# Optimization experiments

Measured on AMD Instinct MI355X. Metric: run time of the kernel, lower is better.

Reference implementation:

```python
import jax, jax.numpy as jnp
import numpy as np

DIM = 1024
H = 16          # query heads
HKV = 4         # kv heads
HD = DIM // H   # head_dim = 64
B = 8           # equal-length docs
S = 1024        # tokens per doc
N = B * S       # total tokens
ROPE_BASE = 10000.0


def _rms_norm(x, scale):
    eps = jnp.asarray(jnp.finfo(x.dtype).eps, x.dtype)
    inv = jax.lax.rsqrt(jnp.mean(x * x, axis=-1, keepdims=True) + eps)
    return x * inv * scale


def _rope(x, cos, sin):
    # x: [N, h, HD]; cos/sin: [N, 1, HD//2]
    half = x.shape[-1] // 2
    x1, x2 = x[..., :half], x[..., half:]
    return jnp.concatenate((x1 * cos + x2 * sin, -x1 * sin + x2 * cos), axis=-1)


def setup_inputs() -> dict:
    key = jax.random.key(0)
    ks = jax.random.split(key, 8)
    x = jax.random.normal(ks[0], (N, DIM), dtype=jnp.float32)
    Wq = jax.random.normal(ks[1], (DIM, DIM), dtype=jnp.float32) * (DIM ** -0.5)
    Wk = jax.random.normal(ks[2], (HKV * HD, DIM), dtype=jnp.float32) * (DIM ** -0.5)
    Wv = jax.random.normal(ks[3], (HKV * HD, DIM), dtype=jnp.float32) * (DIM ** -0.5)
    Wproj = jax.random.normal(ks[4], (DIM, DIM), dtype=jnp.float32) * (DIM ** -0.5)
    q_gain = jnp.full((H,), 1.0, dtype=jnp.float32)
    q_scale = jnp.asarray(1.0, dtype=jnp.float32)  # q RMSNorm scale
    k_scale = jnp.asarray(1.0, dtype=jnp.float32)  # k RMSNorm scale
    # rotary tables per Rotary.prepare_positions (positions reset per doc)
    cu_seqlens = jnp.arange(B + 1, dtype=jnp.int32) * S
    positions = jnp.tile(jnp.arange(S, dtype=jnp.float32), B)  # [N]
    inv_freq = 1.0 / (ROPE_BASE ** (jnp.arange(0, HD, 2, dtype=jnp.float32) / HD))
    freqs = positions[:, None] * inv_freq[None, :]  # [N, HD//2]
    rotary_cos = jnp.cos(freqs)[:, None, :]
    rotary_sin = jnp.sin(freqs)[:, None, :]
    return {
        "x": x, "Wq": Wq, "Wk": Wk, "Wv": Wv, "Wproj": Wproj,
        "q_gain": q_gain, "q_scale": q_scale, "k_scale": k_scale,
        "rotary_cos": rotary_cos, "rotary_sin": rotary_sin,
        "cu_seqlens": cu_seqlens, "max_doc_len": S,
    }


def reference(x, Wq, Wk, Wv, Wproj, q_gain, q_scale, k_scale,
              rotary_cos, rotary_sin, cu_seqlens, max_doc_len):
    n_tokens, dim = x.shape
    q = (x @ Wq.T).reshape(n_tokens, H, HD)
    k = (x @ Wk.T).reshape(n_tokens, HKV, HD)
    v = (x @ Wv.T).reshape(n_tokens, HKV, HD)
    q = _rms_norm(q, q_scale)
    k = _rms_norm(k, k_scale)
    q = _rope(q, rotary_cos, rotary_sin)
    k = _rope(k, rotary_cos, rotary_sin)
    q = q * q_gain[None, :, None]
    # equal-length docs -> [B, S, h, HD]; GQA: repeat kv heads
    rep = H // HKV
    qb = q.reshape(B, S, H, HD)
    kb = jnp.repeat(k.reshape(B, S, HKV, HD), rep, axis=2)
    vb = jnp.repeat(v.reshape(B, S, HKV, HD), rep, axis=2)
    scale = HD ** -0.5
    scores = jnp.einsum('bqhd,bkhd->bhqk', qb, kb) * scale  # [B,H,S,S]
    causal = jnp.tril(jnp.ones((S, S), dtype=bool))
    scores = jnp.where(causal[None, None], scores, jnp.asarray(-jnp.inf, scores.dtype))
    attn = jax.nn.softmax(scores, axis=-1)
    y = jnp.einsum('bhqk,bkhd->bqhd', attn, vb).reshape(n_tokens, dim)
    return y @ Wproj.T
```

## Files before the change

kernel.cpp:

```cpp
#include <hip/hip_runtime.h>
#include <hip/hip_bf16.h>


typedef __bf16 bf16x8 __attribute__((ext_vector_type(8)));
typedef float f32x4 __attribute__((ext_vector_type(4)));

__device__ __forceinline__ void async16(const void* g, void* l) {
  __builtin_amdgcn_global_load_lds((const __attribute__((address_space(1))) void*)g,
                                   (__attribute__((address_space(3))) void*)l, 16, 0, 0);
}

__device__ __forceinline__ unsigned short f2bfu(float x) {
  __hip_bfloat16 h = __float2bfloat16(x);
  return __builtin_bit_cast(unsigned short, h);
}

__global__ __launch_bounds__(256) void castall(
    const float4* __restrict__ x, const float4* __restrict__ Wq,
    const float4* __restrict__ Wk, const float4* __restrict__ Wv,
    const float4* __restrict__ Wp,
    ushort4* __restrict__ xb, ushort4* __restrict__ w1b, ushort4* __restrict__ wpb) {
  int i = blockIdx.x * 256 + threadIdx.x;
  const float4* src;
  ushort4* dst;
  if (i < 2097152)      { src = x + i;             dst = xb + i; }
  else if (i < 2359296) { src = Wq + (i - 2097152); dst = w1b + (i - 2097152); }
  else if (i < 2424832) { src = Wk + (i - 2359296); dst = w1b + (i - 2097152); }
  else if (i < 2490368) { src = Wv + (i - 2424832); dst = w1b + (i - 2097152); }
  else                  { src = Wp + (i - 2490368); dst = wpb + (i - 2490368); }
  float4 v = *src;
  ushort4 o;
  o.x = f2bfu(v.x); o.y = f2bfu(v.y); o.z = f2bfu(v.z); o.w = f2bfu(v.w);
  *dst = o;
}

__global__ __launch_bounds__(256, 3) void gemm_qkv(
    const __hip_bfloat16* __restrict__ A,
    const __hip_bfloat16* __restrict__ Bm,
    const float* __restrict__ cosb, const float* __restrict__ sinb,
    const float* __restrict__ qgain, const float* __restrict__ qscale,
    const float* __restrict__ kscale,
    __hip_bfloat16* __restrict__ Qo,
    __hip_bfloat16* __restrict__ Ko,
    __hip_bfloat16* __restrict__ Vt)
{
  __shared__ __align__(16) unsigned short As[128 * 32];
  __shared__ __align__(16) unsigned short Bs[128 * 32];
  const int tid = threadIdx.x;
  const int wave = tid >> 6, lane = tid & 63;
  const int quad = lane >> 4, l15 = lane & 15;
  const int bn = blockIdx.x, bm = blockIdx.y;
  const int wm = (wave >> 1) * 64, wn = (wave & 1) * 64;
  const int srow = lane >> 2, scol = (lane & 3) * 8;
  const int K = 1024;

  f32x4 acc[4][4] = {};

  const __hip_bfloat16* Ab = A + (size_t)bm * 128 * K;
  const __hip_bfloat16* Bb = Bm + (size_t)bn * 128 * K;

  for (int kt = 0; kt < K; kt += 32) {
    __syncthreads();
#pragma unroll
    for (int c = 0; c < 2; c++) {
      const int ch = wave * 2 + c;
      async16(Ab + (size_t)(ch * 16 + srow) * K + kt + scol, &As[ch * 512]);
      async16(Bb + (size_t)(ch * 16 + srow) * K + kt + scol, &Bs[ch * 512]);
    }
    __syncthreads();
    bf16x8 af[4], bfr[4];
#pragma unroll
    for (int mt = 0; mt < 4; mt++)
      af[mt] = *(const bf16x8*)&As[(wm + mt * 16 + l15) * 32 + quad * 8];
#pragma unroll
    for (int nt = 0; nt < 4; nt++)
      bfr[nt] = *(const bf16x8*)&Bs[(wn + nt * 16 + l15) * 32 + quad * 8];
#pragma unroll
    for (int mt = 0; mt < 4; mt++)
#pragma unroll
      for (int nt = 0; nt < 4; nt++)
        acc[mt][nt] = __builtin_amdgcn_mfma_f32_16x16x32_bf16(af[mt], bfr[nt], acc[mt][nt], 0, 0, 0);
  }

  const int hg = bn * 2 + (wn >> 6);
  const int tokbase = bm * 128 + wm;

  if (hg >= 20) {
    const int hv = hg - 20;
    const int bb = tokbase >> 10;
    const int sbase = (tokbase & 1023) + quad * 4;
    unsigned short* vt = (unsigned short*)Vt;
#pragma unroll
    for (int nt = 0; nt < 4; nt++) {
      const size_t rowoff = ((size_t)((bb * 4 + hv) * 64 + nt * 16 + l15)) * 1024;
#pragma unroll
      for (int mt = 0; mt < 4; mt++) {
        ushort4 pk;
        unsigned short* pp = (unsigned short*)&pk;
#pragma unroll
        for (int r = 0; r < 4; r++) pp[r] = f2bfu(acc[mt][nt][r]);
        *(ushort4*)&vt[rowoff + sbase + mt * 16] = pk;
      }
    }
  } else {
    const bool isq = hg < 16;
    const float scale = isq ? qscale[0] : kscale[0];
    const float gain = isq ? qgain[hg] : 1.0f;
    const float sg = scale * gain;
#pragma unroll
    for (int mt = 0; mt < 4; mt++) {
      float inv[4];
#pragma unroll
      for (int r = 0; r < 4; r++) {
        float ss = acc[mt][0][r] * acc[mt][0][r] + acc[mt][1][r] * acc[mt][1][r] +
                   acc[mt][2][r] * acc[mt][2][r] + acc[mt][3][r] * acc[mt][3][r];
#pragma unroll
        for (int off = 1; off < 16; off <<= 1) ss += __shfl_xor(ss, off);
        inv[r] = rsqrtf(ss * (1.0f / 64.0f) + 1.1920929e-07f) * sg;
      }
#pragma unroll
      for (int r = 0; r < 4; r++) {
        const int tok = tokbase + mt * 16 + quad * 4 + r;
        const float c0 = cosb[tok * 32 + l15], c1 = cosb[tok * 32 + 16 + l15];
        const float s0 = sinb[tok * 32 + l15], s1 = sinb[tok * 32 + 16 + l15];
        const float v0 = acc[mt][0][r] * inv[r];
        const float v1 = acc[mt][1][r] * inv[r];
        const float v2 = acc[mt][2][r] * inv[r];
        const float v3 = acc[mt][3][r] * inv[r];
        const float o0 = v0 * c0 + v2 * s0;
        const float o1 = v1 * c1 + v3 * s1;
        const float o2 = -v0 * s0 + v2 * c0;
        const float o3 = -v1 * s1 + v3 * c1;
        __hip_bfloat16* base = isq ? (Qo + (size_t)tok * 1024 + hg * 64)
                                   : (Ko + (size_t)tok * 256 + (hg - 16) * 64);
        base[l15]      = __float2bfloat16(o0);
        base[16 + l15] = __float2bfloat16(o1);
        base[32 + l15] = __float2bfloat16(o2);
        base[48 + l15] = __float2bfloat16(o3);
      }
    }
  }
}

__global__ __launch_bounds__(256, 4) void gemm_p(
    const __hip_bfloat16* __restrict__ A,
    const __hip_bfloat16* __restrict__ Bm,
    float* __restrict__ C)
{
  __shared__ __align__(16) unsigned short As[128 * 32];
  __shared__ __align__(16) unsigned short Bs[64 * 32];
  const int tid = threadIdx.x;
  const int wave = tid >> 6, lane = tid & 63;
  const int quad = lane >> 4, l15 = lane & 15;
  const int bn = blockIdx.x, bm = blockIdx.y;
  const int wm = wave * 32;
  const int srow = lane >> 2, scol = (lane & 3) * 8;
  const int K = 1024;

  f32x4 acc[2][4] = {};

  const __hip_bfloat16* Ab = A + (size_t)bm * 128 * K;
  const __hip_bfloat16* Bb = Bm + (size_t)bn * 64 * K;

  for (int kt = 0; kt < K; kt += 32) {
    __syncthreads();
#pragma unroll
    for (int c = 0; c < 2; c++) {
      const int ch = wave * 2 + c;
      async16(Ab + (size_t)(ch * 16 + srow) * K + kt + scol, &As[ch * 512]);
    }
    async16(Bb + (size_t)(wave * 16 + srow) * K + kt + scol, &Bs[wave * 512]);
    __syncthreads();
    bf16x8 af[2], bfr[4];
#pragma unroll
    for (int mt = 0; mt < 2; mt++)
      af[mt] = *(const bf16x8*)&As[(wm + mt * 16 + l15) * 32 + quad * 8];
#pragma unroll
    for (int nt = 0; nt < 4; nt++)
      bfr[nt] = *(const bf16x8*)&Bs[(nt * 16 + l15) * 32 + quad * 8];
#pragma unroll
    for (int mt = 0; mt < 2; mt++)
#pragma unroll
      for (int nt = 0; nt < 4; nt++)
        acc[mt][nt] = __builtin_amdgcn_mfma_f32_16x16x32_bf16(af[mt], bfr[nt], acc[mt][nt], 0, 0, 0);
  }

#pragma unroll
  for (int mt = 0; mt < 2; mt++)
#pragma unroll
    for (int nt = 0; nt < 4; nt++)
#pragma unroll
      for (int r = 0; r < 4; r++) {
        const int row = bm * 128 + wm + mt * 16 + quad * 4 + r;
        const int col = bn * 64 + nt * 16 + l15;
        C[(size_t)row * 1024 + col] = acc[mt][nt][r];
      }
}

__global__ __launch_bounds__(256, 3) void attn(
    const __hip_bfloat16* __restrict__ Q,
    const __hip_bfloat16* __restrict__ Kk,
    const __hip_bfloat16* __restrict__ Vt,
    __hip_bfloat16* __restrict__ Y)
{
  __shared__ __align__(16) unsigned short Kb[2][4096];
  __shared__ __align__(16) unsigned short Vb[2][4096];
  __shared__ __align__(16) unsigned short Pm[4][32 * 72];
  __shared__ float Lsh[4][32];

  const int xx = blockIdx.x;
  const int qh = (xx & 1) ? (xx >> 1) : (31 - (xx >> 1));
  const int kvh = blockIdx.y, b = blockIdx.z;
  const int tid = threadIdx.x;
  const int wave = tid >> 6, lane = tid & 63;
  const int quad = lane >> 4, l15 = lane & 15;
  const int h = kvh * 4 + wave;
  const int tok0 = b * 1024 + qh * 32;
  const int m0 = (qh & 1) * 32;
  const int nkt = (qh >> 1) + 1;

  const int srow = lane >> 2;
  const int scol = (lane & 3) * 8;

  bf16x8 qf[2][2];
#pragma unroll
  for (int mt = 0; mt < 2; mt++)
#pragma unroll
    for (int kc = 0; kc < 2; kc++)
      qf[mt][kc] = *(const bf16x8*)(Q + (size_t)(tok0 + mt * 16 + l15) * 1024 +
                                    h * 64 + kc * 32 + quad * 8);

  auto issue = [&](int kt, unsigned short* Ks, unsigned short* Vs) {
#pragma unroll
    for (int c = 0; c < 4; c++) {
      const int ch = wave * 4 + c;
      const int v = ch >> 3;
      const int ch8 = ch & 7;
      const int kc = ch8 >> 2, grp = ch8 & 3;
      if (v == 0)
        async16(Kk + (size_t)(b * 1024 + kt * 64 + grp * 16 + srow) * 256 + kvh * 64 + kc * 32 + scol,
                Ks + kc * 2048 + grp * 512 + lane * 8);
      else
        async16(Vt + ((size_t)((b * 4 + kvh) * 64 + grp * 16 + srow)) * 1024 + kt * 64 + kc * 32 + scol,
                Vs + kc * 2048 + grp * 512 + lane * 8);
    }
  };

  issue(0, Kb[0], Vb[0]);

  f32x4 of[2][4] = {};
  float lsum[2] = {0.0f, 0.0f};
  const float scl2 = 0.125f * 1.44269504089f;
  unsigned short* Pw = Pm[wave];

  for (int kt = 0; kt < nkt; kt++) {
    __syncthreads();
    if (kt + 1 < nkt) issue(kt + 1, Kb[(kt + 1) & 1], Vb[(kt + 1) & 1]);
    const unsigned short* Ks = Kb[kt & 1];
    const unsigned short* Vs = Vb[kt & 1];

    f32x4 sf[4][2] = {};
#pragma unroll
    for (int kc = 0; kc < 2; kc++) {
#pragma unroll
      for (int kk = 0; kk < 4; kk++) {
        const bf16x8 kf = *(const bf16x8*)&Ks[kc * 2048 + (kk * 16 + l15) * 32 + quad * 8];
#pragma unroll
        for (int mt = 0; mt < 2; mt++)
          sf[kk][mt] = __builtin_amdgcn_mfma_f32_16x16x32_bf16(kf, qf[mt][kc], sf[kk][mt], 0, 0, 0);
      }
    }

    const bool diag = (kt == (qh >> 1));
#pragma unroll
    for (int mt = 0; mt < 2; mt++) {
#pragma unroll
      for (int kk = 0; kk < 4; kk++) {
        ushort4 pk;
        unsigned short* pp = (unsigned short*)&pk;
#pragma unroll
        for (int r = 0; r < 4; r++) {
          float p;
          if (diag && (kk * 16 + quad * 4 + r) > (m0 + mt * 16 + l15)) {
            p = 0.0f;
          } else {
            p = __builtin_amdgcn_exp2f(sf[kk][mt][r] * scl2);
          }
          lsum[mt] += p;
          pp[r] = f2bfu(p);
        }
        *(ushort4*)&Pw[(mt * 16 + l15) * 72 + kk * 16 + quad * 4] = pk;
      }
    }

    asm volatile("s_waitcnt lgkmcnt(0)" ::: "memory");

#pragma unroll
    for (int kc = 0; kc < 2; kc++) {
#pragma unroll
      for (int mt = 0; mt < 2; mt++) {
        const bf16x8 ap = *(const bf16x8*)&Pw[(mt * 16 + l15) * 72 + kc * 32 + quad * 8];
#pragma unroll
        for (int dt = 0; dt < 4; dt++) {
          const bf16x8 bv = *(const bf16x8*)&Vs[kc * 2048 + (dt * 16 + l15) * 32 + quad * 8];
          of[mt][dt] = __builtin_amdgcn_mfma_f32_16x16x32_bf16(ap, bv, of[mt][dt], 0, 0, 0);
        }
      }
    }
  }

#pragma unroll
  for (int mt = 0; mt < 2; mt++) {
    float l = lsum[mt];
    l += __shfl_xor(l, 16);
    l += __shfl_xor(l, 32);
    Lsh[wave][mt * 16 + l15] = l;
  }
  asm volatile("s_waitcnt lgkmcnt(0)" ::: "memory");

#pragma unroll
  for (int mt = 0; mt < 2; mt++)
#pragma unroll
    for (int r = 0; r < 4; r++) {
      const float rcp = 1.0f / Lsh[wave][mt * 16 + quad * 4 + r];
      const int row = tok0 + mt * 16 + quad * 4 + r;
#pragma unroll
      for (int dt = 0; dt < 4; dt++)
        Y[(size_t)row * 1024 + h * 64 + dt * 16 + l15] = __float2bfloat16(of[mt][dt][r] * rcp);
    }
}

extern "C" void kernel_launch(void* const* d_in, const int* in_sizes, int n_in,
                              void* d_out, int out_size, void* d_ws, size_t ws_size,
                              hipStream_t stream) {
  const float* x      = (const float*)d_in[0];
  const float* Wq     = (const float*)d_in[1];
  const float* Wk     = (const float*)d_in[2];
  const float* Wv     = (const float*)d_in[3];
  const float* Wp     = (const float*)d_in[4];
  const float* qgain  = (const float*)d_in[5];
  const float* qscale = (const float*)d_in[6];
  const float* kscale = (const float*)d_in[7];
  const float* cosb   = (const float*)d_in[8];
  const float* sinb   = (const float*)d_in[9];
  float* out = (float*)d_out;
  char* ws = (char*)d_ws;

  __hip_bfloat16* xb  = (__hip_bfloat16*)(ws);
  __hip_bfloat16* w1b = (__hip_bfloat16*)(ws + 16777216);
  __hip_bfloat16* wpb = (__hip_bfloat16*)(ws + 19922944);
  __hip_bfloat16* qb  = (__hip_bfloat16*)(ws + 22020096);
  __hip_bfloat16* kb  = (__hip_bfloat16*)(ws + 38797312);
  __hip_bfloat16* vtb = (__hip_bfloat16*)(ws + 42991616);
  __hip_bfloat16* yb  = (__hip_bfloat16*)(ws + 47185920);

  castall<<<10752, 256, 0, stream>>>((const float4*)x, (const float4*)Wq, (const float4*)Wk,
                                     (const float4*)Wv, (const float4*)Wp,
                                     (ushort4*)xb, (ushort4*)w1b, (ushort4*)wpb);

  gemm_qkv<<<dim3(12, 64), 256, 0, stream>>>(xb, w1b, cosb, sinb, qgain, qscale, kscale,
                                             qb, kb, vtb);

  attn<<<dim3(32, 4, 8), 256, 0, stream>>>(qb, kb, vtb, yb);

  gemm_p<<<dim3(16, 64), 256, 0, stream>>>(yb, wpb, out);
}
```

Baseline: 225.4 us.

## Use 64-row query tiles with 8 waves sharing each K/V tile in attention

```diff
diff --git a/kernel.cpp b/kernel.cpp
--- a/kernel.cpp
+++ b/kernel.cpp
@@ -197,7 +197,7 @@
       }
 }
 
-__global__ __launch_bounds__(256, 3) void attn(
+__global__ __launch_bounds__(512, 6) void attn(
     const __hip_bfloat16* __restrict__ Q,
     const __hip_bfloat16* __restrict__ Kk,
     const __hip_bfloat16* __restrict__ Vt,
@@ -205,19 +205,18 @@
 {
   __shared__ __align__(16) unsigned short Kb[2][4096];
   __shared__ __align__(16) unsigned short Vb[2][4096];
-  __shared__ __align__(16) unsigned short Pm[4][32 * 72];
-  __shared__ float Lsh[4][32];
+  __shared__ __align__(16) unsigned short Pm[8][16 * 72];
+  __shared__ float Lsh[8][32];
 
   const int xx = blockIdx.x;
-  const int qh = (xx & 1) ? (xx >> 1) : (31 - (xx >> 1));
+  const int qt = (xx & 1) ? (xx >> 1) : (15 - (xx >> 1));
   const int kvh = blockIdx.y, b = blockIdx.z;
   const int tid = threadIdx.x;
   const int wave = tid >> 6, lane = tid & 63;
   const int quad = lane >> 4, l15 = lane & 15;
-  const int h = kvh * 4 + wave;
-  const int tok0 = b * 1024 + qh * 32;
-  const int m0 = (qh & 1) * 32;
-  const int nkt = (qh >> 1) + 1;
+  const int h = kvh * 4 + (wave >> 1);
+  const int m0 = (wave & 1) * 32;
+  const int tok0 = b * 1024 + qt * 64;
 
   const int srow = lane >> 2;
   const int scol = (lane & 3) * 8;
@@ -227,13 +226,13 @@
   for (int mt = 0; mt < 2; mt++)
 #pragma unroll
     for (int kc = 0; kc < 2; kc++)
-      qf[mt][kc] = *(const bf16x8*)(Q + (size_t)(tok0 + mt * 16 + l15) * 1024 +
+      qf[mt][kc] = *(const bf16x8*)(Q + (size_t)(tok0 + m0 + mt * 16 + l15) * 1024 +
                                     h * 64 + kc * 32 + quad * 8);
 
   auto issue = [&](int kt, unsigned short* Ks, unsigned short* Vs) {
 #pragma unroll
-    for (int c = 0; c < 4; c++) {
-      const int ch = wave * 4 + c;
+    for (int c = 0; c < 2; c++) {
+      const int ch = wave * 2 + c;
       const int v = ch >> 3;
       const int ch8 = ch & 7;
       const int kc = ch8 >> 2, grp = ch8 & 3;
@@ -253,29 +252,23 @@
   const float scl2 = 0.125f * 1.44269504089f;
   unsigned short* Pw = Pm[wave];
 
-  for (int kt = 0; kt < nkt; kt++) {
-    __syncthreads();
-    if (kt + 1 < nkt) issue(kt + 1, Kb[(kt + 1) & 1], Vb[(kt + 1) & 1]);
+  for (int kt = 0; kt <= qt; kt++) {
+    __syncthreads();
+    if (kt < qt) issue(kt + 1, Kb[(kt + 1) & 1], Vb[(kt + 1) & 1]);
     const unsigned short* Ks = Kb[kt & 1];
     const unsigned short* Vs = Vb[kt & 1];
-
-    f32x4 sf[4][2] = {};
-#pragma unroll
-    for (int kc = 0; kc < 2; kc++) {
+    const bool diag = (kt == qt);
+
+#pragma unroll
+    for (int mt = 0; mt < 2; mt++) {
 #pragma unroll
       for (int kk = 0; kk < 4; kk++) {
-        const bf16x8 kf = *(const bf16x8*)&Ks[kc * 2048 + (kk * 16 + l15) * 32 + quad * 8];
-#pragma unroll
-        for (int mt = 0; mt < 2; mt++)
-          sf[kk][mt] = __builtin_amdgcn_mfma_f32_16x16x32_bf16(kf, qf[mt][kc], sf[kk][mt], 0, 0, 0);
-      }
-    }
-
-    const bool diag = (kt == (qh >> 1));
-#pragma unroll
-    for (int mt = 0; mt < 2; mt++) {
-#pragma unroll
-      for (int kk = 0; kk < 4; kk++) {
+        f32x4 s = {};
+#pragma unroll
+        for (int kc = 0; kc < 2; kc++) {
+          const bf16x8 kf = *(const bf16x8*)&Ks[kc * 2048 + (kk * 16 + l15) * 32 + quad * 8];
+          s = __builtin_amdgcn_mfma_f32_16x16x32_bf16(kf, qf[mt][kc], s, 0, 0, 0);
+        }
         ushort4 pk;
         unsigned short* pp = (unsigned short*)&pk;
 #pragma unroll
@@ -284,22 +277,17 @@
           if (diag && (kk * 16 + quad * 4 + r) > (m0 + mt * 16 + l15)) {
             p = 0.0f;
           } else {
-            p = __builtin_amdgcn_exp2f(sf[kk][mt][r] * scl2);
+            p = __builtin_amdgcn_exp2f(s[r] * scl2);
           }
           lsum[mt] += p;
           pp[r] = f2bfu(p);
         }
-        *(ushort4*)&Pw[(mt * 16 + l15) * 72 + kk * 16 + quad * 4] = pk;
-      }
-    }
-
-    asm volatile("s_waitcnt lgkmcnt(0)" ::: "memory");
-
-#pragma unroll
-    for (int kc = 0; kc < 2; kc++) {
-#pragma unroll
-      for (int mt = 0; mt < 2; mt++) {
-        const bf16x8 ap = *(const bf16x8*)&Pw[(mt * 16 + l15) * 72 + kc * 32 + quad * 8];
+        *(ushort4*)&Pw[l15 * 72 + kk * 16 + quad * 4] = pk;
+      }
+
+#pragma unroll
+      for (int kc = 0; kc < 2; kc++) {
+        const bf16x8 ap = *(const bf16x8*)&Pw[l15 * 72 + kc * 32 + quad * 8];
 #pragma unroll
         for (int dt = 0; dt < 4; dt++) {
           const bf16x8 bv = *(const bf16x8*)&Vs[kc * 2048 + (dt * 16 + l15) * 32 + quad * 8];
@@ -323,7 +311,7 @@
 #pragma unroll
     for (int r = 0; r < 4; r++) {
       const float rcp = 1.0f / Lsh[wave][mt * 16 + quad * 4 + r];
-      const int row = tok0 + mt * 16 + quad * 4 + r;
+      const int row = tok0 + m0 + mt * 16 + quad * 4 + r;
 #pragma unroll
       for (int dt = 0; dt < 4; dt++)
         Y[(size_t)row * 1024 + h * 64 + dt * 16 + l15] = __float2bfloat16(of[mt][dt][r] * rcp);
@@ -361,7 +349,7 @@
   gemm_qkv<<<dim3(12, 64), 256, 0, stream>>>(xb, w1b, cosb, sinb, qgain, qscale, kscale,
                                              qb, kb, vtb);
 
-  attn<<<dim3(32, 4, 8), 256, 0, stream>>>(qb, kb, vtb, yb);
+  attn<<<dim3(16, 4, 8), 512, 0, stream>>>(qb, kb, vtb, yb);
 
   gemm_p<<<dim3(16, 64), 256, 0, stream>>>(yb, wpb, out);
 }
```

After: 347.7 us. +54.3%, slower.
